# Kernel tuning notes

Hardware: AMD Instinct MI355X
Metric: run time of the kernel (lower is better)

## Reference

```python
import jax, jax.numpy as jnp
import numpy as np

N_NODES = 100_000
N_EDGES = 1_600_000
IN_F = 256
HID = 256
OUT_F = 256
BN_EPS = 1e-5


def make_quaternion_mul(kernel):
    # kernel: [d, 4m] -> hamilton: [4d, 4m]
    dim = kernel.shape[1] // 4
    r, i, j, k = jnp.split(kernel, 4, axis=1)
    r2 = jnp.concatenate([r, -i, -j, -k], axis=0)
    i2 = jnp.concatenate([i, r, -k, j], axis=0)
    j2 = jnp.concatenate([j, k, r, -i], axis=0)
    k2 = jnp.concatenate([k, -j, i, r], axis=0)
    return jnp.concatenate([r2, i2, j2, k2], axis=1)


def setup_inputs() -> dict:
    key = jax.random.key(0)
    ks = jax.random.split(key, 6)
    x = jax.random.normal(ks[0], (N_NODES, IN_F), dtype=jnp.float32)
    rows = jax.random.randint(ks[1], (N_EDGES,), 0, N_NODES, dtype=jnp.int32)
    cols = jax.random.randint(ks[2], (N_EDGES,), 0, N_NODES, dtype=jnp.int32)
    edge_vals = jax.random.uniform(ks[3], (N_EDGES,), dtype=jnp.float32)
    stdv1 = np.sqrt(6.0 / (IN_F // 4 + HID))
    weight1 = jax.random.uniform(ks[4], (IN_F // 4, HID), dtype=jnp.float32,
                                 minval=-stdv1, maxval=stdv1)
    stdv2 = np.sqrt(6.0 / (HID // 4 + OUT_F))
    weight2 = jax.random.uniform(ks[5], (HID // 4, OUT_F), dtype=jnp.float32,
                                 minval=-stdv2, maxval=stdv2)
    gamma = jnp.ones((HID,), dtype=jnp.float32)
    beta = jnp.zeros((HID,), dtype=jnp.float32)
    return {"x": x, "rows": rows, "cols": cols, "edge_vals": edge_vals,
            "weight1": weight1, "weight2": weight2, "gamma": gamma, "beta": beta}


def reference(x, rows, cols, edge_vals, weight1, weight2, gamma, beta):
    hamilton1 = make_quaternion_mul(weight1)  # [IN_F, HID]
    hamilton2 = make_quaternion_mul(weight2)  # [HID, OUT_F]
    # spmm: new_x[r] = sum_e adj[r,c]*x[c] over edges (r=rows, c=cols)
    gathered = edge_vals[:, None] * x[cols]               # [E, IN_F]
    new_x = jax.ops.segment_sum(gathered, rows, num_segments=N_NODES)
    out1 = new_x @ hamilton1                              # [N, HID]
    # BatchNorm1d (training mode): biased batch stats over nodes
    mean = jnp.mean(out1, axis=0)
    var = jnp.mean(jnp.square(out1 - mean), axis=0)
    out1 = (out1 - mean) * jax.lax.rsqrt(var + BN_EPS) * gamma + beta
    out1 = jnp.tanh(out1)
    return out1 @ hamilton2                               # [N, OUT_F]
```

## Files before the change

### kernel.cpp

```cpp
#include <hip/hip_runtime.h>
#include <hip/hip_bf16.h>
#include <math.h>


#define FDIM 256
#define NREP 32
#define CH 2048

typedef __attribute__((ext_vector_type(8))) short bf16x8;
typedef __attribute__((ext_vector_type(4))) float f32x4;

static __device__ inline short f2bf(float x) {
    __hip_bfloat16 h = __float2bfloat16(x);
    return *reinterpret_cast<short*>(&h);
}
static __device__ inline float bf2f(unsigned short u) {
    union { unsigned int i; float f; } c;
    c.i = ((unsigned int)u) << 16;
    return c.f;
}
static __device__ inline float fast_tanh(float x) {
    float e = __expf(2.f * x);
    return 1.f - 2.f * __builtin_amdgcn_rcpf(e + 1.f);
}

static __device__ void build_hfrag(const float* __restrict__ w, ushort* __restrict__ hf,
                                   int t) {
    const int   comp_t[16] = {0,1,2,3,  1,0,3,2,  2,3,0,1,  3,2,1,0};
    const float sign_t[16] = {1,1,1,1, -1,1,1,-1, -1,-1,1,1, -1,1,-1,1};
    int f = t >> 6, lane = t & 63;
    int tile = f >> 3, kk = f & 7;
    int col = tile * 16 + (lane & 15);
    int b = col >> 6, q = col & 63;
    ushort o[8];
#pragma unroll
    for (int j = 0; j < 8; ++j) {
        int k = kk * 32 + ((lane >> 4) << 3) + j;
        int a = k >> 6, p = k & 63;
        int ab = a * 4 + b;
        float v = sign_t[ab] * w[p * 256 + comp_t[ab] * 64 + q];
        o[j] = (ushort)f2bf(v);
    }
    *(ushort4*)(hf + (size_t)t * 8)     = make_ushort4(o[0], o[1], o[2], o[3]);
    *(ushort4*)(hf + (size_t)t * 8 + 4) = make_ushort4(o[4], o[5], o[6], o[7]);
}

__global__ __launch_bounds__(256) void k_initp1(const float* __restrict__ w1,
                                                const float* __restrict__ w2,
                                                ushort* __restrict__ h1f,
                                                ushort* __restrict__ h2f,
                                                float* __restrict__ statsR,
                                                const int* __restrict__ rows,
                                                int* __restrict__ CM,
                                                int E, int nchunk, int NB) {
    int b = blockIdx.x;
    if (b < 32) {
        build_hfrag(w1, h1f, b * 256 + threadIdx.x);
        return;
    }
    if (b < 64) {
        build_hfrag(w2, h2f, (b - 32) * 256 + threadIdx.x);
        return;
    }
    if (b < 80) {
        int slot = (b - 64) * 256 + threadIdx.x;
        *(float4*)(statsR + slot * 4) = make_float4(0.f, 0.f, 0.f, 0.f);
        return;
    }
    __shared__ int lc[256];
    int t = threadIdx.x, c = b - 80;
    lc[t] = 0;
    __syncthreads();
#pragma unroll
    for (int i = 0; i < 8; ++i) {
        int e = c * CH + i * 256 + t;
        if (e < E) atomicAdd(&lc[rows[e] >> 9], 1);
    }
    __syncthreads();
    if (t < NB) CM[t * nchunk + c] = lc[t];
}

__global__ __launch_bounds__(256) void k_p2(const int* __restrict__ CM,
                                            int* __restrict__ PO,
                                            int* __restrict__ BT, int nchunk) {
    __shared__ int ts[256];
    int t = threadIdx.x, b = blockIdx.x;
    int base = b * nchunk;
    int lex[4], s = 0;
#pragma unroll
    for (int i = 0; i < 4; ++i) {
        int c = t * 4 + i;
        int v = (c < nchunk) ? CM[base + c] : 0;
        lex[i] = s;
        s += v;
    }
    ts[t] = s;
    __syncthreads();
    for (int off = 1; off < 256; off <<= 1) {
        int v = (t >= off) ? ts[t - off] : 0;
        __syncthreads();
        ts[t] += v;
        __syncthreads();
    }
    int excl = ts[t] - s;
#pragma unroll
    for (int i = 0; i < 4; ++i) {
        int c = t * 4 + i;
        if (c < nchunk) PO[base + c] = excl + lex[i];
    }
    if (t == 255) BT[b] = ts[255];
}

__global__ __launch_bounds__(256) void k_p3(const int* __restrict__ rows,
                                            const int* __restrict__ cols,
                                            const float* __restrict__ vals,
                                            const int* __restrict__ PO,
                                            const int* __restrict__ BT,
                                            uint2* __restrict__ tmp2,
                                            int E, int nchunk, int NB) {
    __shared__ int sBB[256];
    __shared__ int sPO[256];
    __shared__ int sLC[256];
    int t = threadIdx.x, c = blockIdx.x;
    int own = (t < NB) ? BT[t] : 0;
    sBB[t] = own;
    sPO[t] = (t < NB) ? PO[t * nchunk + c] : 0;
    sLC[t] = 0;
    __syncthreads();
    for (int off = 1; off < 256; off <<= 1) {
        int v = (t >= off) ? sBB[t - off] : 0;
        __syncthreads();
        sBB[t] += v;
        __syncthreads();
    }
    sBB[t] -= own;
    __syncthreads();
#pragma unroll
    for (int i = 0; i < 8; ++i) {
        int e = c * CH + i * 256 + t;
        if (e < E) {
            int r = rows[e];
            int b = r >> 9;
            int rank = atomicAdd(&sLC[b], 1);
            int pos = sBB[b] + sPO[b] + rank;
            int iv = (int)(vals[e] * 32768.0f);
            tmp2[pos] = make_uint2((unsigned int)cols[e] | ((unsigned int)iv << 17),
                                   (unsigned int)r);
        }
    }
}

__global__ __launch_bounds__(1024) void k_p4(const uint2* __restrict__ tmp2,
                                             const int* __restrict__ BT,
                                             unsigned int* __restrict__ ew,
                                             uint2* __restrict__ offs2,
                                             int N, int NB) {
    __shared__ int sBB[256];
    __shared__ int sH[512];
    __shared__ int sHp[512];
    __shared__ int sOp[512];
    __shared__ int sC[512];
    int t = threadIdx.x, b = blockIdx.x;
    int own = 0;
    if (t < 256) {
        own = (t < NB) ? BT[t] : 0;
        sBB[t] = own;
    }
    __syncthreads();
    for (int off = 1; off < 256; off <<= 1) {
        int v = (t < 256 && t >= off) ? sBB[t - off] : 0;
        __syncthreads();
        if (t < 256) sBB[t] += v;
        __syncthreads();
    }
    if (t < 256) sBB[t] -= own;
    if (t < 512) sH[t] = 0;
    __syncthreads();
    const int base = sBB[b];
    const int basePad = sBB[b] + b * 4096;
    const int nE = BT[b];
    const int rbase = b << 9;
    for (int i = t; i < nE; i += 1024)
        atomicAdd(&sH[(int)tmp2[base + i].y - rbase], 1);
    __syncthreads();
    if (t < 512) {
        int hp = (sH[t] + 7) & ~7;
        sHp[t] = hp;
        sOp[t] = hp;
    }
    __syncthreads();
    for (int off = 1; off < 512; off <<= 1) {
        int v = (t < 512 && t >= off) ? sOp[t - off] : 0;
        __syncthreads();
        if (t < 512) sOp[t] += v;
        __syncthreads();
    }
    if (t < 512) {
        sOp[t] -= sHp[t];
        int r = rbase + t;
        if (r < N) offs2[r] = make_uint2((unsigned int)(basePad + sOp[t]),
                                         (unsigned int)sHp[t]);
        sC[t] = 0;
    }
    __syncthreads();
    for (int i = t; i < nE; i += 1024) {
        uint2 u = tmp2[base + i];
        int lr = (int)u.y - rbase;
        int p = atomicAdd(&sC[lr], 1);
        ew[basePad + sOp[lr] + p] = u.x;
    }
    if (t < 512) {
        int e0 = basePad + sOp[t] + sH[t];
        int e1 = basePad + sOp[t] + sHp[t];
        for (int e = e0; e < e1; ++e) ew[e] = 0u;
    }
}

__global__ __launch_bounds__(256) void k_gemm1(const float* __restrict__ X,
                                               const ushort* __restrict__ Bf,
                                               ushort* __restrict__ Y, int N) {
    __shared__ float4 lds4[2048];
    ushort* lds = (ushort*)lds4;
    const int t = threadIdx.x;
    const int w = t >> 6, lane = t & 63;
    const int r0 = blockIdx.x * 64 + w * 16;
    const int q = (lane >> 4) & 3, l = lane & 15;
    const int kbase = q * 8;
    const int rA = min(r0 + l, N - 1);

    bf16x8 af[8];
#pragma unroll
    for (int kk = 0; kk < 8; ++kk) {
        const float* p = X + (size_t)rA * 256 + kk * 32 + kbase;
        float4 v0 = *(const float4*)p;
        float4 v1 = *(const float4*)(p + 4);
        bf16x8 a;
        a[0] = f2bf(v0.x); a[1] = f2bf(v0.y); a[2] = f2bf(v0.z); a[3] = f2bf(v0.w);
        a[4] = f2bf(v1.x); a[5] = f2bf(v1.y); a[6] = f2bf(v1.z); a[7] = f2bf(v1.w);
        af[kk] = a;
    }

    for (int g = 0; g < 4; ++g) {
        {
            const float4* s4 = (const float4*)(Bf + (size_t)g * 16384);
#pragma unroll
            for (int i = 0; i < 8; ++i) lds4[i * 256 + t] = s4[i * 256 + t];
        }
        __syncthreads();

        f32x4 acc[4];
#pragma unroll
        for (int tg = 0; tg < 4; ++tg) acc[tg] = (f32x4){0.f, 0.f, 0.f, 0.f};

#pragma unroll
        for (int tg = 0; tg < 4; ++tg)
#pragma unroll
            for (int kk = 0; kk < 8; ++kk) {
                bf16x8 b = *(const bf16x8*)(lds + ((tg * 8 + kk) * 64 + lane) * 8);
                acc[tg] = __builtin_amdgcn_mfma_f32_16x16x32_bf16(af[kk], b, acc[tg], 0, 0, 0);
            }
        __syncthreads();

        {
            ushort* cw = lds + w * 1024;
#pragma unroll
            for (int tg = 0; tg < 4; ++tg)
#pragma unroll
                for (int j = 0; j < 4; ++j)
                    cw[(q * 4 + j) * 64 + tg * 16 + l] = (ushort)f2bf(acc[tg][j]);
            int gcol0 = g * 64;
        }
        __syncthreads();
        {
            int gcol0 = g * 64;
#pragma unroll
            for (int p = 0; p < 2; ++p) {
                uint4 rd = *(const uint4*)(lds + w * 1024 + p * 512 + lane * 8);
                int row = r0 + p * 8 + (lane >> 3);
                int col = gcol0 + (lane & 7) * 8;
                if (row < N) *(uint4*)(Y + (size_t)row * 256 + col) = rd;
            }
        }
        __syncthreads();
    }
}

__global__ __launch_bounds__(256) void k_spmm(const ushort* __restrict__ Y,
                                              const uint2* __restrict__ offs2,
                                              const unsigned int* __restrict__ ew,
                                              ushort* __restrict__ O,
                                              float* __restrict__ statsR,
                                              int n, int W, int half) {
    __shared__ float ls_s[4][128];
    __shared__ float ls_q[4][128];
    const int tid = threadIdx.x;
    const int w = tid >> 6, lane = tid & 63;
    const int gw = blockIdx.x * 4 + w;
    const int fb = half * 128 + lane * 2;

    float s0 = 0.f, s1 = 0.f;
    float q0 = 0.f, q1 = 0.f;

    for (int k = 0; k < 4; ++k) {
        int row = gw + k * W;
        bool ok = row < n;
        int r = ok ? row : 0;
        uint2 bc = offs2[r];
        int cnt = ok ? (int)bc.y : 0;
        int g = cnt >> 3;
        const unsigned int* ep = ew + bc.x;

        float a0 = 0.f, a1 = 0.f;
        unsigned int wv[8];
        if (g > 0) {
#pragma unroll
            for (int i = 0; i < 8; ++i) wv[i] = ep[i];
        }
        for (int gi = 0; gi < g; ++gi) {
            unsigned int wn[8];
            bool more = (gi + 1) < g;
            if (more) {
#pragma unroll
                for (int i = 0; i < 8; ++i) wn[i] = ep[(gi + 1) * 8 + i];
            }
#pragma unroll
            for (int i = 0; i < 8; ++i) {
                unsigned int wd = wv[i];
                int c = (int)(wd & 0x1FFFFu);
                float v = (float)(wd >> 17) * (1.0f / 32768.0f);
                ushort2 yv = *(const ushort2*)(Y + (size_t)c * 256 + fb);
                a0 = fmaf(v, bf2f(yv.x), a0);
                a1 = fmaf(v, bf2f(yv.y), a1);
            }
            if (more) {
#pragma unroll
                for (int i = 0; i < 8; ++i) wv[i] = wn[i];
            }
        }
        if (ok) {
            ushort2 o = make_ushort2((ushort)f2bf(a0), (ushort)f2bf(a1));
            *(ushort2*)(O + (size_t)r * 512 + fb) = o;
        }
        s0 += a0; q0 = fmaf(a0, a0, q0);
        s1 += a1; q1 = fmaf(a1, a1, q1);
    }

    int rep = blockIdx.x & (NREP - 1);
    *(float2*)&ls_s[w][lane * 2] = make_float2(s0, s1);
    *(float2*)&ls_q[w][lane * 2] = make_float2(q0, q1);
    __syncthreads();
    if (tid < 128) {
        float sv = ls_s[0][tid] + ls_s[1][tid] + ls_s[2][tid] + ls_s[3][tid];
        float qv = ls_q[0][tid] + ls_q[1][tid] + ls_q[2][tid] + ls_q[3][tid];
        atomicAdd(&statsR[rep * 256 + half * 128 + tid], sv);
        atomicAdd(&statsR[NREP * 256 + rep * 256 + half * 128 + tid], qv);
    }
}

__global__ __launch_bounds__(256) void k_gemm2(void* __restrict__ Av,
                                               const ushort* __restrict__ Bf,
                                               const float* __restrict__ statsR,
                                               const float* __restrict__ gamma,
                                               const float* __restrict__ beta, int N) {
    __shared__ float4 lds4[2048];
    ushort* lds = (ushort*)lds4;
    __shared__ float sscl[256], sshf[256];
    const int t = threadIdx.x;
    const int w = t >> 6, lane = t & 63;
    const int r0 = blockIdx.x * 64 + w * 16;
    const int q = (lane >> 4) & 3, l = lane & 15;
    const int kbase = q * 8;
    const int rA = min(r0 + l, N - 1);

    {
        float s = 0.f, qq = 0.f;
#pragma unroll
        for (int i = 0; i < NREP; ++i) {
            s += statsR[i * 256 + t];
            qq += statsR[NREP * 256 + i * 256 + t];
        }
        float invn = 1.0f / (float)N;
        float mean = s * invn;
        float var = qq * invn - mean * mean;
        float inv = rsqrtf(var + 1e-5f);
        float gg = gamma[t] * inv;
        sscl[t] = gg;
        sshf[t] = beta[t] - mean * gg;
        __syncthreads();
    }

    const ushort* X = (const ushort*)Av;
    bf16x8 af[8];
#pragma unroll
    for (int kk = 0; kk < 8; ++kk) {
        const ushort* p = X + (size_t)rA * 512 + kk * 32 + kbase;
        ushort4 u0 = *(const ushort4*)p;
        ushort4 u1 = *(const ushort4*)(p + 4);
        float4 s0 = *(const float4*)&sscl[kk * 32 + kbase];
        float4 s1 = *(const float4*)&sscl[kk * 32 + kbase + 4];
        float4 h0 = *(const float4*)&sshf[kk * 32 + kbase];
        float4 h1 = *(const float4*)&sshf[kk * 32 + kbase + 4];
        bf16x8 a;
        a[0] = f2bf(fast_tanh(fmaf(bf2f(u0.x), s0.x, h0.x)));
        a[1] = f2bf(fast_tanh(fmaf(bf2f(u0.y), s0.y, h0.y)));
        a[2] = f2bf(fast_tanh(fmaf(bf2f(u0.z), s0.z, h0.z)));
        a[3] = f2bf(fast_tanh(fmaf(bf2f(u0.w), s0.w, h0.w)));
        a[4] = f2bf(fast_tanh(fmaf(bf2f(u1.x), s1.x, h1.x)));
        a[5] = f2bf(fast_tanh(fmaf(bf2f(u1.y), s1.y, h1.y)));
        a[6] = f2bf(fast_tanh(fmaf(bf2f(u1.z), s1.z, h1.z)));
        a[7] = f2bf(fast_tanh(fmaf(bf2f(u1.w), s1.w, h1.w)));
        af[kk] = a;
    }

    float* Cf = (float*)Av;
    for (int g = 0; g < 4; ++g) {
        {
            const float4* s4 = (const float4*)(Bf + (size_t)g * 16384);
#pragma unroll
            for (int i = 0; i < 8; ++i) lds4[i * 256 + t] = s4[i * 256 + t];
        }
        __syncthreads();

        f32x4 acc[4];
#pragma unroll
        for (int tg = 0; tg < 4; ++tg) acc[tg] = (f32x4){0.f, 0.f, 0.f, 0.f};

#pragma unroll
        for (int tg = 0; tg < 4; ++tg)
#pragma unroll
            for (int kk = 0; kk < 8; ++kk) {
                bf16x8 b = *(const bf16x8*)(lds + ((tg * 8 + kk) * 64 + lane) * 8);
                acc[tg] = __builtin_amdgcn_mfma_f32_16x16x32_bf16(af[kk], b, acc[tg], 0, 0, 0);
            }
        __syncthreads();

        {
            float* cw = (float*)lds4 + w * 1024;
#pragma unroll
            for (int tg = 0; tg < 4; ++tg)
#pragma unroll
                for (int j = 0; j < 4; ++j)
                    cw[(q * 4 + j) * 64 + tg * 16 + l] = acc[tg][j];
        }
        __syncthreads();
        {
            int gcol0 = g * 64;
#pragma unroll
            for (int p = 0; p < 4; ++p) {
                f32x4 rd = *(const f32x4*)((float*)lds4 + w * 1024 + p * 256 + lane * 4);
                int row = r0 + p * 4 + (lane >> 4);
                int col = gcol0 + (lane & 15) * 4;
                if (row < N)
                    __builtin_nontemporal_store(rd, (f32x4*)(Cf + (size_t)row * 256 + col));
            }
        }
        __syncthreads();
    }
}

extern "C" void kernel_launch(void* const* d_in, const int* in_sizes, int n_in,
                              void* d_out, int out_size, void* d_ws, size_t ws_size,
                              hipStream_t stream) {
    const float* x     = (const float*)d_in[0];
    const int* rows    = (const int*)d_in[1];
    const int* cols    = (const int*)d_in[2];
    const float* evin  = (const float*)d_in[3];
    const float* w1    = (const float*)d_in[4];
    const float* w2    = (const float*)d_in[5];
    const float* gamma = (const float*)d_in[6];
    const float* beta  = (const float*)d_in[7];
    float* out = (float*)d_out;

    const int N = in_sizes[0] / FDIM;
    const int E = in_sizes[1];
    const int NB = (N + 511) >> 9;
    const int nchunk = (E + CH - 1) / CH;

    char* ws = (char*)d_ws;
    size_t o = 0;
    auto alloc = [&](size_t bytes) -> char* {
        char* p = ws + o;
        o += (bytes + 255) & ~(size_t)255;
        return p;
    };
    ushort* h1f  = (ushort*)alloc(128 * 64 * 8 * 2);
    ushort* h2f  = (ushort*)alloc(128 * 64 * 8 * 2);
    ushort* y    = (ushort*)alloc((size_t)N * 256 * 2);
    float* statsR = (float*)alloc(2 * NREP * 256 * 4);
    int*   CM    = (int*)alloc((size_t)NB * nchunk * 4);
    int*   PO    = (int*)alloc((size_t)NB * nchunk * 4);
    int*   BT    = (int*)alloc(256 * 4);
    uint2* tmp2  = (uint2*)alloc((size_t)E * 8);
    unsigned int* ewp = (unsigned int*)alloc(((size_t)E + (size_t)NB * 4096 + 16) * 4);
    uint2* offs2 = (uint2*)alloc((size_t)N * 8);

    k_initp1<<<80 + nchunk, 256, 0, stream>>>(w1, w2, h1f, h2f, statsR,
                                              rows, CM, E, nchunk, NB);
    k_p2<<<NB, 256, 0, stream>>>(CM, PO, BT, nchunk);
    k_p3<<<nchunk, 256, 0, stream>>>(rows, cols, evin, PO, BT, tmp2, E, nchunk, NB);
    k_p4<<<NB, 1024, 0, stream>>>(tmp2, BT, ewp, offs2, N, NB);

    int gblk = (N + 63) / 64;
    k_gemm1<<<gblk, 256, 0, stream>>>(x, h1f, y, N);
    int W = (N + 3) / 4;
    int sblk = (W + 3) / 4;
    k_spmm<<<sblk, 256, 0, stream>>>(y, offs2, ewp, (ushort*)out, statsR, N, W, 0);
    k_spmm<<<sblk, 256, 0, stream>>>(y, offs2, ewp, (ushort*)out, statsR, N, W, 1);
    k_gemm2<<<gblk, 256, 0, stream>>>(out, h2f, statsR, gamma, beta, N);
}
```

Measured before the change: 243.6 us.

## Switch pipeline to fp16, merge SpMM halves, accumulate with packed half FMA

Converts intermediate storage and MFMA operands from bf16 to fp16 and stores edge weights as fp16 bits in place of fixed-point. The two half-feature SpMM launches become one, with each lane covering four features through packed __hfma2 accumulation and readfirstlane-broadcast edge words. The aim is to halve the passes over the edge list, cut per-edge ALU work and widen the gathers. The risk is fp16 range and precision loss when accumulating in half, which could overflow or drift on high-degree rows.

```diff
diff --git a/kernel.cpp b/kernel.cpp
--- a/kernel.cpp
+++ b/kernel.cpp
@@ -1,5 +1,6 @@
 #include <hip/hip_runtime.h>
 #include <hip/hip_bf16.h>
+#include <hip/hip_fp16.h>
 #include <math.h>
 
 
@@ -7,17 +8,15 @@
 #define NREP 32
 #define CH 2048
 
-typedef __attribute__((ext_vector_type(8))) short bf16x8;
+typedef __attribute__((ext_vector_type(8))) _Float16 f16x8;
 typedef __attribute__((ext_vector_type(4))) float f32x4;
 
-static __device__ inline short f2bf(float x) {
-    __hip_bfloat16 h = __float2bfloat16(x);
-    return *reinterpret_cast<short*>(&h);
-}
-static __device__ inline float bf2f(unsigned short u) {
-    union { unsigned int i; float f; } c;
-    c.i = ((unsigned int)u) << 16;
-    return c.f;
+static __device__ inline ushort f2h_bits(float x) {
+    _Float16 h = (_Float16)x;
+    return __builtin_bit_cast(unsigned short, h);
+}
+static __device__ inline float h2f(ushort u) {
+    return (float)__builtin_bit_cast(_Float16, u);
 }
 static __device__ inline float fast_tanh(float x) {
     float e = __expf(2.f * x);
@@ -39,7 +38,7 @@
         int a = k >> 6, p = k & 63;
         int ab = a * 4 + b;
         float v = sign_t[ab] * w[p * 256 + comp_t[ab] * 64 + q];
-        o[j] = (ushort)f2bf(v);
+        o[j] = f2h_bits(v);
     }
     *(ushort4*)(hf + (size_t)t * 8)     = make_ushort4(o[0], o[1], o[2], o[3]);
     *(ushort4*)(hf + (size_t)t * 8 + 4) = make_ushort4(o[4], o[5], o[6], o[7]);
@@ -143,8 +142,8 @@
             int b = r >> 9;
             int rank = atomicAdd(&sLC[b], 1);
             int pos = sBB[b] + sPO[b] + rank;
-            int iv = (int)(vals[e] * 32768.0f);
-            tmp2[pos] = make_uint2((unsigned int)cols[e] | ((unsigned int)iv << 17),
+            unsigned int hv = f2h_bits(vals[e]);
+            tmp2[pos] = make_uint2((unsigned int)cols[e] | (hv << 17),
                                    (unsigned int)r);
         }
     }
@@ -228,15 +227,17 @@
     const int kbase = q * 8;
     const int rA = min(r0 + l, N - 1);
 
-    bf16x8 af[8];
+    f16x8 af[8];
 #pragma unroll
     for (int kk = 0; kk < 8; ++kk) {
         const float* p = X + (size_t)rA * 256 + kk * 32 + kbase;
         float4 v0 = *(const float4*)p;
         float4 v1 = *(const float4*)(p + 4);
-        bf16x8 a;
-        a[0] = f2bf(v0.x); a[1] = f2bf(v0.y); a[2] = f2bf(v0.z); a[3] = f2bf(v0.w);
-        a[4] = f2bf(v1.x); a[5] = f2bf(v1.y); a[6] = f2bf(v1.z); a[7] = f2bf(v1.w);
+        f16x8 a;
+        a[0] = (_Float16)v0.x; a[1] = (_Float16)v0.y;
+        a[2] = (_Float16)v0.z; a[3] = (_Float16)v0.w;
+        a[4] = (_Float16)v1.x; a[5] = (_Float16)v1.y;
+        a[6] = (_Float16)v1.z; a[7] = (_Float16)v1.w;
         af[kk] = a;
     }
 
@@ -256,8 +257,8 @@
         for (int tg = 0; tg < 4; ++tg)
 #pragma unroll
             for (int kk = 0; kk < 8; ++kk) {
-                bf16x8 b = *(const bf16x8*)(lds + ((tg * 8 + kk) * 64 + lane) * 8);
-                acc[tg] = __builtin_amdgcn_mfma_f32_16x16x32_bf16(af[kk], b, acc[tg], 0, 0, 0);
+                f16x8 b = *(const f16x8*)(lds + ((tg * 8 + kk) * 64 + lane) * 8);
+                acc[tg] = __builtin_amdgcn_mfma_f32_16x16x32_f16(af[kk], b, acc[tg], 0, 0, 0);
             }
         __syncthreads();
 
@@ -267,8 +268,7 @@
             for (int tg = 0; tg < 4; ++tg)
 #pragma unroll
                 for (int j = 0; j < 4; ++j)
-                    cw[(q * 4 + j) * 64 + tg * 16 + l] = (ushort)f2bf(acc[tg][j]);
-            int gcol0 = g * 64;
+                    cw[(q * 4 + j) * 64 + tg * 16 + l] = f2h_bits(acc[tg][j]);
         }
         __syncthreads();
         {
@@ -290,16 +290,15 @@
                                               const unsigned int* __restrict__ ew,
                                               ushort* __restrict__ O,
                                               float* __restrict__ statsR,
-                                              int n, int W, int half) {
-    __shared__ float ls_s[4][128];
-    __shared__ float ls_q[4][128];
+                                              int n, int W) {
+    __shared__ float ls_s[4][256];
+    __shared__ float ls_q[4][256];
     const int tid = threadIdx.x;
     const int w = tid >> 6, lane = tid & 63;
     const int gw = blockIdx.x * 4 + w;
-    const int fb = half * 128 + lane * 2;
-
-    float s0 = 0.f, s1 = 0.f;
-    float q0 = 0.f, q1 = 0.f;
+
+    float s0 = 0.f, s1 = 0.f, s2 = 0.f, s3 = 0.f;
+    float q0 = 0.f, q1 = 0.f, q2 = 0.f, q3 = 0.f;
 
     for (int k = 0; k < 4; ++k) {
         int row = gw + k * W;
@@ -310,7 +309,8 @@
         int g = cnt >> 3;
         const unsigned int* ep = ew + bc.x;
 
-        float a0 = 0.f, a1 = 0.f;
+        __half2 a01 = __builtin_bit_cast(__half2, 0u);
+        __half2 a23 = __builtin_bit_cast(__half2, 0u);
         unsigned int wv[8];
         if (g > 0) {
 #pragma unroll
@@ -325,12 +325,13 @@
             }
 #pragma unroll
             for (int i = 0; i < 8; ++i) {
-                unsigned int wd = wv[i];
-                int c = (int)(wd & 0x1FFFFu);
-                float v = (float)(wd >> 17) * (1.0f / 32768.0f);
-                ushort2 yv = *(const ushort2*)(Y + (size_t)c * 256 + fb);
-                a0 = fmaf(v, bf2f(yv.x), a0);
-                a1 = fmaf(v, bf2f(yv.y), a1);
+                unsigned int wd = (unsigned int)__builtin_amdgcn_readfirstlane((int)wv[i]);
+                unsigned int c = wd & 0x1FFFFu;
+                unsigned int hv = wd >> 17;
+                __half2 vv = __builtin_bit_cast(__half2, hv | (hv << 16));
+                uint2 u = *(const uint2*)(Y + (size_t)c * 256 + lane * 4);
+                a01 = __hfma2(__builtin_bit_cast(__half2, u.x), vv, a01);
+                a23 = __hfma2(__builtin_bit_cast(__half2, u.y), vv, a23);
             }
             if (more) {
 #pragma unroll
@@ -338,23 +339,26 @@
             }
         }
         if (ok) {
-            ushort2 o = make_ushort2((ushort)f2bf(a0), (ushort)f2bf(a1));
-            *(ushort2*)(O + (size_t)r * 512 + fb) = o;
-        }
-        s0 += a0; q0 = fmaf(a0, a0, q0);
-        s1 += a1; q1 = fmaf(a1, a1, q1);
+            uint2 o = make_uint2(__builtin_bit_cast(unsigned int, a01),
+                                 __builtin_bit_cast(unsigned int, a23));
+            *(uint2*)(O + (size_t)r * 512 + lane * 4) = o;
+        }
+        float2 f01 = __half22float2(a01);
+        float2 f23 = __half22float2(a23);
+        s0 += f01.x; q0 = fmaf(f01.x, f01.x, q0);
+        s1 += f01.y; q1 = fmaf(f01.y, f01.y, q1);
+        s2 += f23.x; q2 = fmaf(f23.x, f23.x, q2);
+        s3 += f23.y; q3 = fmaf(f23.y, f23.y, q3);
     }
 
     int rep = blockIdx.x & (NREP - 1);
-    *(float2*)&ls_s[w][lane * 2] = make_float2(s0, s1);
-    *(float2*)&ls_q[w][lane * 2] = make_float2(q0, q1);
-    __syncthreads();
-    if (tid < 128) {
-        float sv = ls_s[0][tid] + ls_s[1][tid] + ls_s[2][tid] + ls_s[3][tid];
-        float qv = ls_q[0][tid] + ls_q[1][tid] + ls_q[2][tid] + ls_q[3][tid];
-        atomicAdd(&statsR[rep * 256 + half * 128 + tid], sv);
-        atomicAdd(&statsR[NREP * 256 + rep * 256 + half * 128 + tid], qv);
-    }
+    *(float4*)&ls_s[w][lane * 4] = make_float4(s0, s1, s2, s3);
+    *(float4*)&ls_q[w][lane * 4] = make_float4(q0, q1, q2, q3);
+    __syncthreads();
+    float sv = ls_s[0][tid] + ls_s[1][tid] + ls_s[2][tid] + ls_s[3][tid];
+    float qv = ls_q[0][tid] + ls_q[1][tid] + ls_q[2][tid] + ls_q[3][tid];
+    atomicAdd(&statsR[rep * 256 + tid], sv);
+    atomicAdd(&statsR[NREP * 256 + rep * 256 + tid], qv);
 }
 
 __global__ __launch_bounds__(256) void k_gemm2(void* __restrict__ Av,
@@ -390,7 +394,7 @@
     }
 
     const ushort* X = (const ushort*)Av;
-    bf16x8 af[8];
+    f16x8 af[8];
 #pragma unroll
     for (int kk = 0; kk < 8; ++kk) {
         const ushort* p = X + (size_t)rA * 512 + kk * 32 + kbase;
@@ -400,15 +404,15 @@
         float4 s1 = *(const float4*)&sscl[kk * 32 + kbase + 4];
         float4 h0 = *(const float4*)&sshf[kk * 32 + kbase];
         float4 h1 = *(const float4*)&sshf[kk * 32 + kbase + 4];
-        bf16x8 a;
-        a[0] = f2bf(fast_tanh(fmaf(bf2f(u0.x), s0.x, h0.x)));
-        a[1] = f2bf(fast_tanh(fmaf(bf2f(u0.y), s0.y, h0.y)));
-        a[2] = f2bf(fast_tanh(fmaf(bf2f(u0.z), s0.z, h0.z)));
-        a[3] = f2bf(fast_tanh(fmaf(bf2f(u0.w), s0.w, h0.w)));
-        a[4] = f2bf(fast_tanh(fmaf(bf2f(u1.x), s1.x, h1.x)));
-        a[5] = f2bf(fast_tanh(fmaf(bf2f(u1.y), s1.y, h1.y)));
-        a[6] = f2bf(fast_tanh(fmaf(bf2f(u1.z), s1.z, h1.z)));
-        a[7] = f2bf(fast_tanh(fmaf(bf2f(u1.w), s1.w, h1.w)));
+        f16x8 a;
+        a[0] = (_Float16)fast_tanh(fmaf(h2f(u0.x), s0.x, h0.x));
+        a[1] = (_Float16)fast_tanh(fmaf(h2f(u0.y), s0.y, h0.y));
+        a[2] = (_Float16)fast_tanh(fmaf(h2f(u0.z), s0.z, h0.z));
+        a[3] = (_Float16)fast_tanh(fmaf(h2f(u0.w), s0.w, h0.w));
+        a[4] = (_Float16)fast_tanh(fmaf(h2f(u1.x), s1.x, h1.x));
+        a[5] = (_Float16)fast_tanh(fmaf(h2f(u1.y), s1.y, h1.y));
+        a[6] = (_Float16)fast_tanh(fmaf(h2f(u1.z), s1.z, h1.z));
+        a[7] = (_Float16)fast_tanh(fmaf(h2f(u1.w), s1.w, h1.w));
         af[kk] = a;
     }
 
@@ -429,8 +433,8 @@
         for (int tg = 0; tg < 4; ++tg)
 #pragma unroll
             for (int kk = 0; kk < 8; ++kk) {
-                bf16x8 b = *(const bf16x8*)(lds + ((tg * 8 + kk) * 64 + lane) * 8);
-                acc[tg] = __builtin_amdgcn_mfma_f32_16x16x32_bf16(af[kk], b, acc[tg], 0, 0, 0);
+                f16x8 b = *(const f16x8*)(lds + ((tg * 8 + kk) * 64 + lane) * 8);
+                acc[tg] = __builtin_amdgcn_mfma_f32_16x16x32_f16(af[kk], b, acc[tg], 0, 0, 0);
             }
         __syncthreads();
 
@@ -504,7 +508,6 @@
     k_gemm1<<<gblk, 256, 0, stream>>>(x, h1f, y, N);
     int W = (N + 3) / 4;
     int sblk = (W + 3) / 4;
-    k_spmm<<<sblk, 256, 0, stream>>>(y, offs2, ewp, (ushort*)out, statsR, N, W, 0);
-    k_spmm<<<sblk, 256, 0, stream>>>(y, offs2, ewp, (ushort*)out, statsR, N, W, 1);
+    k_spmm<<<sblk, 256, 0, stream>>>(y, offs2, ewp, (ushort*)out, statsR, N, W);
     k_gemm2<<<gblk, 256, 0, stream>>>(out, h2f, statsR, gamma, beta, N);
 }
```

Measured after the change: 246.6 us. Within noise of the previous version (+1.2%).
